# Kernel tuning notes

Hardware: AMD Instinct MI355X
Metric: run time of the kernel (lower is better)

Reference implementation:

```python
import jax, jax.numpy as jnp
import numpy as np

B, S, DMODEL, NHEAD = 2, 2048, 1024, 16
DK = DMODEL // NHEAD
INITRANGE = 0.1


def setup_inputs() -> dict:
    key = jax.random.key(0)
    kq, kk, kv, kwq, kwk, kwv, kwo = jax.random.split(key, 7)
    unif = lambda k, shape: jax.random.uniform(k, shape, jnp.float32, -INITRANGE, INITRANGE)
    return {
        "Q": jax.random.normal(kq, (B, S, DMODEL), jnp.float32),
        "K": jax.random.normal(kk, (B, S, DMODEL), jnp.float32),
        "V": jax.random.normal(kv, (B, S, DMODEL), jnp.float32),
        "WQ": unif(kwq, (NHEAD, DMODEL, DK)),
        "WK": unif(kwk, (NHEAD, DMODEL, DK)),
        "WV": unif(kwv, (NHEAD, DMODEL, DK)),
        "WO": unif(kwo, (NHEAD * DK, DMODEL)),
    }


def reference(Q, K, V, WQ, WK, WV, WO):
    dk = WQ.shape[-1]
    # per-head projections: [B,S,D] x [H,D,dk] -> [B,H,S,dk]
    Qi = jnp.einsum('bsd,hdk->bhsk', Q, WQ)
    Ki = jnp.einsum('bsd,hdk->bhsk', K, WK)
    Vi = jnp.einsum('bsd,hdk->bhsk', V, WV)
    scale = 1.0 / jnp.sqrt(jnp.asarray(dk, Qi.dtype))
    # full attention matrix [B,H,S,S] (faithful to the hand-rolled module; dropout in eval mode)
    attn = jax.nn.softmax(jnp.einsum('bhsk,bhtk->bhst', Qi, Ki) * scale, axis=-1)
    headi = jnp.einsum('bhst,bhtk->bhsk', attn, Vi)  # [B,H,S,dk]
    b, h, s, _ = headi.shape
    # NOTE: original does a raw reshape of contiguous (B,H,S,dk) -> (B,S,H*dk),
    # which mixes head and sequence axes in memory order. jnp row-major reshape
    # reproduces exactly the same element layout.
    out = headi.reshape(b, s, h * dk) @ WO  # [B,S,DMODEL]
    return out
```

## Files before the change

kernel.cpp:

```cpp
#include <hip/hip_runtime.h>
#include <hip/hip_bf16.h>
#include <stdint.h>

typedef unsigned short u16;
typedef unsigned int u32;
typedef __attribute__((ext_vector_type(4))) float f32x4;
typedef __attribute__((ext_vector_type(16))) float f32x16;
typedef __attribute__((ext_vector_type(8))) short bf16x8;
typedef __attribute__((ext_vector_type(4))) unsigned int u32x4;
typedef __attribute__((ext_vector_type(2))) unsigned int u32x2;

#define DEV __device__ __forceinline__

DEV u16 f2bf(float f) {
  union { float f; uint32_t u; } v; v.f = f;
  uint32_t u = v.u;
  return (u16)((u + 0x7fffu + ((u >> 16) & 1u)) >> 16);
}
DEV float bf2f(u16 h) {
  union { uint32_t u; float f; } v; v.u = ((uint32_t)h) << 16;
  return v.f;
}

DEV u32 cvtpk(float a, float b) {
  u32 r;
  asm("v_cvt_pk_bf16_f32 %0, %1, %2" : "=v"(r) : "v"(a), "v"(b));
  return r;
}

DEV void plswap(u32& a, u32& b) {
  asm("v_permlane32_swap_b32 %0, %1" : "+v"(a), "+v"(b));
}

DEV float fexp2(float x) {
  float r;
  asm("v_exp_f32 %0, %1" : "=v"(r) : "v"(x));
  return r;
}

DEV void gload_lds16(const u16* g, u16* l) {
  __builtin_amdgcn_global_load_lds(
      (const __attribute__((address_space(1))) void*)g,
      (__attribute__((address_space(3))) void*)l, 16, 0, 0);
}

__global__ __launch_bounds__(256) void prep_kernel(
    const float* __restrict__ Q, const float* __restrict__ K, const float* __restrict__ V,
    const float* __restrict__ WQ, const float* __restrict__ WK, const float* __restrict__ WV,
    const float* __restrict__ WO,
    u16* __restrict__ Qb, u16* __restrict__ Kb, u16* __restrict__ Vb,
    u16* __restrict__ Wt, u16* __restrict__ Wot) {
  const int i = blockIdx.x * 256 + threadIdx.x;
#pragma unroll
  for (int it = 0; it < 3; ++it) {
    int idx = it * 1048576 + i;
    int which = idx >> 20, j = idx & 1048575;
    const float* src = which == 0 ? Q : (which == 1 ? K : V);
    u16* dst = which == 0 ? Qb : (which == 1 ? Kb : Vb);
    float4 v = ((const float4*)src)[j];
    u32x2 pk;
    pk[0] = (u32)f2bf(v.x) | ((u32)f2bf(v.y) << 16);
    pk[1] = (u32)f2bf(v.z) | ((u32)f2bf(v.w) << 16);
    *(u32x2*)(dst + (size_t)j * 4) = pk;
  }
#pragma unroll
  for (int it = 0; it < 4; ++it) {
    int idx = it * 1048576 + i;
    if (idx < 3145728) {
      int p = idx >> 20, r = idx & 1048575;
      int n = r >> 10, d = r & 1023;
      int h = n >> 6, k = n & 63;
      const float* src = p == 0 ? WQ : (p == 1 ? WK : WV);
      Wt[idx] = f2bf(src[(h * 1024 + d) * 64 + k]);
    } else {
      int j = idx - 3145728;
      int c = j >> 10, k = j & 1023;
      Wot[j] = f2bf(WO[k * 1024 + c]);
    }
  }
}

template <int OUT_BF16>
__global__ __launch_bounds__(256, 2) void gemm_kernel(const u16* __restrict__ A,
                                                      const u16* __restrict__ Bt,
                                                      void* __restrict__ Cout) {
  __shared__ __align__(16) u16 Alds[128 * 64];
  __shared__ __align__(16) u16 Blds[128 * 64];
  const size_t zo = blockIdx.z;
  A += zo * 4194304;
  Bt += zo * 1048576;
  const int tid = threadIdx.x;
  const int l = tid & 63, w = tid >> 6;
  const int wm = w >> 1, wn = w & 1;
  const int d = blockIdx.x + 32 * blockIdx.y;
  const int orig = (d & 7) * 32 + (d >> 3);
  const int tileM = (orig & 31) * 128, tileN = (orig >> 5) * 128;
  const int lr = l >> 3, lch = l & 7;

  f32x4 acc[4][4] = {};

  for (int kt = 0; kt < 16; ++kt) {
    const int k0 = kt * 64;
#pragma unroll
    for (int i = 0; i < 4; ++i) {
      int r = i * 32 + w * 8 + lr;
      int sch = lch ^ (r & 7);
      gload_lds16(A + (size_t)(tileM + r) * 1024 + k0 + sch * 8, Alds + i * 2048 + w * 512);
      gload_lds16(Bt + (size_t)(tileN + r) * 1024 + k0 + sch * 8, Blds + i * 2048 + w * 512);
    }
    __syncthreads();
    bf16x8 af[4][2], bfr[4][2];
#pragma unroll
    for (int m = 0; m < 4; ++m) {
#pragma unroll
      for (int kk = 0; kk < 2; ++kk) {
        int row = wm * 64 + m * 16 + (l & 15);
        int ch = ((l >> 4) + kk * 4) ^ (row & 7);
        af[m][kk] = *(const bf16x8*)(Alds + row * 64 + ch * 8);
        int rowb = wn * 64 + m * 16 + (l & 15);
        int chb = ((l >> 4) + kk * 4) ^ (rowb & 7);
        bfr[m][kk] = *(const bf16x8*)(Blds + rowb * 64 + chb * 8);
      }
    }
#pragma unroll
    for (int m = 0; m < 4; ++m)
#pragma unroll
      for (int n = 0; n < 4; ++n)
#pragma unroll
        for (int kk = 0; kk < 2; ++kk)
          acc[m][n] = __builtin_amdgcn_mfma_f32_16x16x32_bf16(af[m][kk], bfr[n][kk], acc[m][n], 0, 0, 0);
    __syncthreads();
  }
#pragma unroll
  for (int m = 0; m < 4; ++m) {
    int row0 = tileM + wm * 64 + m * 16 + ((l >> 4) << 2);
#pragma unroll
    for (int n = 0; n < 4; ++n) {
      int col = tileN + wn * 64 + n * 16 + (l & 15);
#pragma unroll
      for (int q = 0; q < 4; ++q) {
        if (OUT_BF16)
          ((u16*)Cout)[zo * 4194304 + (size_t)(row0 + q) * 1024 + col] = f2bf(acc[m][n][q]);
        else
          ((float*)Cout)[(size_t)(row0 + q) * 1024 + col] = acc[m][n][q];
      }
    }
  }
}

__global__ __launch_bounds__(256) void transposeV_kernel(const u16* __restrict__ Vi,
                                                         u16* __restrict__ Vt) {
  __shared__ __align__(16) u16 tl[64][72];
  const int tid = threadIdx.x;
  const int st = blockIdx.x * 64;
  const int bh = blockIdx.y;
  const int b = bh >> 4, h = bh & 15;
#pragma unroll
  for (int i = 0; i < 2; ++i) {
    int idx = i * 256 + tid;
    int s = idx >> 3, ch = idx & 7;
    const u16* src = Vi + (size_t)(b * 2048 + st + s) * 1024 + h * 64 + ch * 8;
    u32x2 a = *(const u32x2*)src;
    u32x2 bb = *(const u32x2*)(src + 4);
    *(u32x2*)&tl[s][ch * 8] = a;
    *(u32x2*)&tl[s][ch * 8 + 4] = bb;
  }
  __syncthreads();
#pragma unroll
  for (int i = 0; i < 2; ++i) {
    int idx = i * 256 + tid;
    int dk = idx >> 3, ch = idx & 7;
    u32x4 outv;
    u16* tp = (u16*)&outv;
#pragma unroll
    for (int j = 0; j < 8; ++j) tp[j] = tl[ch * 8 + j][dk];
    *(u32x4*)(Vt + ((size_t)bh * 64 + dk) * 2048 + st + ch * 8) = outv;
  }
}

__global__ __launch_bounds__(256, 4) void attn_kernel(const u16* __restrict__ Qi,
                                                      const u16* __restrict__ Ki,
                                                      const u16* __restrict__ Vt,
                                                      u16* __restrict__ Op,
                                                      float* __restrict__ Lp) {
  __shared__ __align__(16) u16 Kl[2][4096];
  __shared__ __align__(16) u16 Vl[2][4096];
  const int tid = threadIdx.x;
  const int l = tid & 63, w = tid >> 6;
  const int lq = l & 31, hi = l >> 5;
  const int lr = l >> 3, lch = l & 7;
  const int dd = blockIdx.x;
  const int orig = (dd & 7) * 128 + (dd >> 3);
  const int bh = orig >> 5;
  const int rem = orig & 31;
  const int qb = rem >> 1, kvh = rem & 1;
  const int b = bh >> 4, h = bh & 15;
  const int qt = qb * 128 + w * 32;
  const int tb = kvh * 1024;

  const u16* Kbase = Ki + (size_t)b * 2048 * 1024 + h * 64;
  const u16* Vbase = Vt + (size_t)bh * 64 * 2048;

  bf16x8 qf[4];
  {
    const u16* qp = Qi + (size_t)(b * 2048 + qt + lq) * 1024 + h * 64 + hi * 8;
#pragma unroll
    for (int s = 0; s < 4; ++s) {
      u32x4 t4 = *(const u32x4*)(qp + s * 16);
      u16* tp = (u16*)&t4;
#pragma unroll
      for (int j = 0; j < 8; ++j) tp[j] = f2bf(bf2f(tp[j]) * 0.1803368867f);
      qf[s] = *(bf16x8*)&t4;
    }
  }

  f32x16 o0 = {}, o1 = {};
  float l_r = 0.f;

  auto STAGE = [&](int bb, int t) {
#pragma unroll
    for (int i = 0; i < 2; ++i) {
      int r = i * 32 + w * 8 + lr;
      int sch = lch ^ (r & 7);
      gload_lds16(Kbase + (size_t)(tb + t * 64 + r) * 1024 + sch * 8,
                  Kl[bb] + i * 2048 + w * 512);
      gload_lds16(Vbase + (size_t)r * 2048 + tb + t * 64 + sch * 8,
                  Vl[bb] + i * 2048 + w * 512);
    }
  };

  STAGE(0, 0);

#pragma unroll 2
  for (int tile = 0; tile < 16; ++tile) {
    const int cur = tile & 1;
    __syncthreads();
    if (tile + 1 < 16) STAGE(cur ^ 1, tile + 1);
    const u16* kl = Kl[cur];
    const u16* vl = Vl[cur];

    f32x16 s0 = {}, s1 = {};
    __builtin_amdgcn_s_setprio(1);
#pragma unroll
    for (int s = 0; s < 4; ++s) {
      int row = lq, c = s * 2 + hi;
      bf16x8 kf = *(const bf16x8*)(kl + row * 64 + (c ^ (row & 7)) * 8);
      s0 = __builtin_amdgcn_mfma_f32_32x32x16_bf16(kf, qf[s], s0, 0, 0, 0);
    }
#pragma unroll
    for (int s = 0; s < 4; ++s) {
      int row = 32 + lq, c = s * 2 + hi;
      bf16x8 kf = *(const bf16x8*)(kl + row * 64 + (c ^ (row & 7)) * 8);
      s1 = __builtin_amdgcn_mfma_f32_32x32x16_bf16(kf, qf[s], s1, 0, 0, 0);
    }
    __builtin_amdgcn_s_setprio(0);

    float rs = 0.f;
    bf16x8 pa[4];
#pragma unroll
    for (int s4 = 0; s4 < 4; ++s4) {
      const int rb = 8 * (s4 & 1);
      float p[8];
#pragma unroll
      for (int j = 0; j < 8; ++j) {
        float sv = (s4 < 2) ? ((const float*)&s0)[rb + j] : ((const float*)&s1)[rb + j];
        p[j] = fexp2(sv);
      }
      rs += ((p[0] + p[1]) + (p[2] + p[3])) + ((p[4] + p[5]) + (p[6] + p[7]));
      u32 w10 = cvtpk(p[0], p[1]);
      u32 w11 = cvtpk(p[2], p[3]);
      u32 w20 = cvtpk(p[4], p[5]);
      u32 w21 = cvtpk(p[6], p[7]);
      plswap(w10, w20);
      plswap(w11, w21);
      u32x4 af;
      af[0] = w10;
      af[1] = w11;
      af[2] = w20;
      af[3] = w21;
      pa[s4] = *(bf16x8*)&af;
    }
    rs += __shfl_xor(rs, 32, 64);
    l_r += rs;

    __builtin_amdgcn_s_setprio(1);
#pragma unroll
    for (int s4 = 0; s4 < 4; ++s4) {
      int rowd = lq, c = s4 * 2 + hi;
      bf16x8 vf = *(const bf16x8*)(vl + rowd * 64 + (c ^ (rowd & 7)) * 8);
      o0 = __builtin_amdgcn_mfma_f32_32x32x16_bf16(pa[s4], vf, o0, 0, 0, 0);
    }
#pragma unroll
    for (int s4 = 0; s4 < 4; ++s4) {
      int rowd = 32 + lq, c = s4 * 2 + hi;
      bf16x8 vf = *(const bf16x8*)(vl + rowd * 64 + (c ^ (rowd & 7)) * 8);
      o1 = __builtin_amdgcn_mfma_f32_32x32x16_bf16(pa[s4], vf, o1, 0, 0, 0);
    }
    __builtin_amdgcn_s_setprio(0);
  }

#pragma unroll
  for (int r = 0; r < 16; ++r) {
    int qr = (r & 3) + 8 * (r >> 2) + 4 * hi;
    u16* hp = Op + (size_t)kvh * 4194304 + ((size_t)bh * 2048 + qt + qr) * 64;
    hp[lq] = f2bf(o0[r]);
    hp[32 + lq] = f2bf(o1[r]);
  }
  if (hi == 0) Lp[(size_t)kvh * 65536 + (size_t)bh * 2048 + qt + lq] = l_r;
}

__global__ __launch_bounds__(256) void combine_kernel(const u16* __restrict__ Op,
                                                      const float* __restrict__ Lp,
                                                      u16* __restrict__ Hd) {
  const int idx = blockIdx.x * 256 + threadIdx.x;
  const int g = idx >> 3, j = idx & 7;
  const float fac = 1.f / (Lp[g] + Lp[65536 + g]);
  const u16* a = Op + (size_t)g * 64 + j * 8;
  const u16* bptr = a + 4194304;
  u32x4 va = *(const u32x4*)a;
  u32x4 vb = *(const u32x4*)bptr;
  const u16* pa = (const u16*)&va;
  const u16* pb = (const u16*)&vb;
  u32x4 outv;
  u16* po = (u16*)&outv;
#pragma unroll
  for (int e = 0; e < 8; ++e) po[e] = f2bf((bf2f(pa[e]) + bf2f(pb[e])) * fac);
  *(u32x4*)(Hd + (size_t)g * 64 + j * 8) = outv;
}

extern "C" void kernel_launch(void* const* d_in, const int* in_sizes, int n_in,
                              void* d_out, int out_size, void* d_ws, size_t ws_size,
                              hipStream_t stream) {
  const float* Q = (const float*)d_in[0];
  const float* K = (const float*)d_in[1];
  const float* V = (const float*)d_in[2];
  const float* WQ = (const float*)d_in[3];
  const float* WK = (const float*)d_in[4];
  const float* WV = (const float*)d_in[5];
  const float* WO = (const float*)d_in[6];
  float* out = (float*)d_out;

  size_t off = 0;
  char* ws = (char*)d_ws;
  auto nxt = [&](size_t n) { void* p = ws + off; off += (n + 255) & ~(size_t)255; return p; };
  u16* Qb = (u16*)nxt(3ull * 4096 * 1024 * 2);
  u16* Qi = (u16*)nxt(3ull * 4096 * 1024 * 2);
  u16* Vtb = (u16*)nxt(4096ull * 1024 * 2);
  u16* Hd = (u16*)nxt(4096ull * 1024 * 2);
  u16* Wt = (u16*)nxt(3ull * 1048576 * 2);
  u16* Wot = (u16*)nxt(1048576ull * 2);
  u16* Ki = Qi + 4194304;
  u16* Vi = Qi + 2 * 4194304;
  u16* Op = Qb;
  float* Lp = (float*)(Qb + 2ull * 4194304);

  prep_kernel<<<4096, 256, 0, stream>>>(Q, K, V, WQ, WK, WV, WO, Qb, Qb + 4194304,
                                        Qb + 2 * 4194304, Wt, Wot);

  gemm_kernel<1><<<dim3(32, 8, 3), 256, 0, stream>>>(Qb, Wt, Qi);

  transposeV_kernel<<<dim3(32, 32), 256, 0, stream>>>(Vi, Vtb);

  attn_kernel<<<1024, 256, 0, stream>>>(Qi, Ki, Vtb, Op, Lp);

  combine_kernel<<<2048, 256, 0, stream>>>(Op, Lp, Hd);

  gemm_kernel<0><<<dim3(32, 8, 1), 256, 0, stream>>>(Hd, Wot, out);
}
```

Baseline: 140.0 us.

## Split attention KV range four ways and tile weight transposes through LDS

The attention kernel now splits each query block's key range into four chunks instead of two, which doubles the grid to 2048 blocks for more parallelism. The fourth partial output goes into the Hd buffer and Lp moves to its own workspace region. The combine kernel now sums four partials. Weight conversion and transposition move out of the prep kernel into a separate LDS-tiled transpose kernel, replacing the strided, uncoalesced gathers. The cost is extra partial-output traffic in combine and one more kernel launch.

```diff
diff --git a/kernel.cpp b/kernel.cpp
--- a/kernel.cpp
+++ b/kernel.cpp
@@ -46,10 +46,7 @@
 
 __global__ __launch_bounds__(256) void prep_kernel(
     const float* __restrict__ Q, const float* __restrict__ K, const float* __restrict__ V,
-    const float* __restrict__ WQ, const float* __restrict__ WK, const float* __restrict__ WV,
-    const float* __restrict__ WO,
-    u16* __restrict__ Qb, u16* __restrict__ Kb, u16* __restrict__ Vb,
-    u16* __restrict__ Wt, u16* __restrict__ Wot) {
+    u16* __restrict__ Qb, u16* __restrict__ Kb, u16* __restrict__ Vb) {
   const int i = blockIdx.x * 256 + threadIdx.x;
 #pragma unroll
   for (int it = 0; it < 3; ++it) {
@@ -63,20 +60,55 @@
     pk[1] = (u32)f2bf(v.z) | ((u32)f2bf(v.w) << 16);
     *(u32x2*)(dst + (size_t)j * 4) = pk;
   }
-#pragma unroll
-  for (int it = 0; it < 4; ++it) {
-    int idx = it * 1048576 + i;
-    if (idx < 3145728) {
-      int p = idx >> 20, r = idx & 1048575;
-      int n = r >> 10, d = r & 1023;
-      int h = n >> 6, k = n & 63;
-      const float* src = p == 0 ? WQ : (p == 1 ? WK : WV);
-      Wt[idx] = f2bf(src[(h * 1024 + d) * 64 + k]);
-    } else {
-      int j = idx - 3145728;
-      int c = j >> 10, k = j & 1023;
-      Wot[j] = f2bf(WO[k * 1024 + c]);
-    }
+}
+
+__global__ __launch_bounds__(256) void transposeW_kernel(
+    const float* __restrict__ WQ, const float* __restrict__ WK, const float* __restrict__ WV,
+    const float* __restrict__ WO, u16* __restrict__ Wt, u16* __restrict__ Wot) {
+  __shared__ __align__(16) u16 tl[64][72];
+  const int tid = threadIdx.x;
+  const int bid = blockIdx.x;
+  const float* src;
+  u16* dst;
+  int rstride;
+  if (bid < 768) {
+    int p = bid >> 8, rest = bid & 255;
+    int h = rest >> 4, dt = rest & 15;
+    const float* W = p == 0 ? WQ : (p == 1 ? WK : WV);
+    src = W + (size_t)(h * 1024 + dt * 64) * 64;
+    dst = Wt + (size_t)p * 1048576 + (size_t)h * 64 * 1024 + dt * 64;
+    rstride = 64;
+  } else {
+    int idx2 = bid - 768;
+    int kt = idx2 >> 4, ct = idx2 & 15;
+    src = WO + (size_t)kt * 64 * 1024 + ct * 64;
+    dst = Wot + (size_t)ct * 64 * 1024 + kt * 64;
+    rstride = 1024;
+  }
+#pragma unroll
+  for (int i = 0; i < 2; ++i) {
+    int idx = i * 256 + tid;
+    int row = idx >> 3, c8 = idx & 7;
+    const float* sp = src + (size_t)row * rstride + c8 * 8;
+    float4 a = *(const float4*)sp;
+    float4 b = *(const float4*)(sp + 4);
+    u32x4 pk;
+    pk[0] = (u32)f2bf(a.x) | ((u32)f2bf(a.y) << 16);
+    pk[1] = (u32)f2bf(a.z) | ((u32)f2bf(a.w) << 16);
+    pk[2] = (u32)f2bf(b.x) | ((u32)f2bf(b.y) << 16);
+    pk[3] = (u32)f2bf(b.z) | ((u32)f2bf(b.w) << 16);
+    *(u32x4*)&tl[row][c8 * 8] = pk;
+  }
+  __syncthreads();
+#pragma unroll
+  for (int i = 0; i < 2; ++i) {
+    int idx = i * 256 + tid;
+    int row2 = idx >> 3, s8 = idx & 7;
+    u32x4 outv;
+    u16* tp = (u16*)&outv;
+#pragma unroll
+    for (int j = 0; j < 8; ++j) tp[j] = tl[s8 * 8 + j][row2];
+    *(u32x4*)(dst + (size_t)row2 * 1024 + s8 * 8) = outv;
   }
 }
 
@@ -182,6 +214,7 @@
                                                       const u16* __restrict__ Ki,
                                                       const u16* __restrict__ Vt,
                                                       u16* __restrict__ Op,
+                                                      u16* __restrict__ Op3,
                                                       float* __restrict__ Lp) {
   __shared__ __align__(16) u16 Kl[2][4096];
   __shared__ __align__(16) u16 Vl[2][4096];
@@ -190,13 +223,13 @@
   const int lq = l & 31, hi = l >> 5;
   const int lr = l >> 3, lch = l & 7;
   const int dd = blockIdx.x;
-  const int orig = (dd & 7) * 128 + (dd >> 3);
-  const int bh = orig >> 5;
-  const int rem = orig & 31;
-  const int qb = rem >> 1, kvh = rem & 1;
+  const int orig = (dd & 7) * 256 + (dd >> 3);
+  const int bh = orig >> 6;
+  const int rem = orig & 63;
+  const int qb = rem >> 2, kvh = rem & 3;
   const int b = bh >> 4, h = bh & 15;
   const int qt = qb * 128 + w * 32;
-  const int tb = kvh * 1024;
+  const int tb = kvh * 512;
 
   const u16* Kbase = Ki + (size_t)b * 2048 * 1024 + h * 64;
   const u16* Vbase = Vt + (size_t)bh * 64 * 2048;
@@ -232,10 +265,10 @@
   STAGE(0, 0);
 
 #pragma unroll 2
-  for (int tile = 0; tile < 16; ++tile) {
+  for (int tile = 0; tile < 8; ++tile) {
     const int cur = tile & 1;
     __syncthreads();
-    if (tile + 1 < 16) STAGE(cur ^ 1, tile + 1);
+    if (tile + 1 < 8) STAGE(cur ^ 1, tile + 1);
     const u16* kl = Kl[cur];
     const u16* vl = Vl[cur];
 
@@ -299,10 +332,11 @@
     __builtin_amdgcn_s_setprio(0);
   }
 
+  u16* opb = (kvh == 3) ? Op3 : (Op + (size_t)kvh * 4194304);
 #pragma unroll
   for (int r = 0; r < 16; ++r) {
     int qr = (r & 3) + 8 * (r >> 2) + 4 * hi;
-    u16* hp = Op + (size_t)kvh * 4194304 + ((size_t)bh * 2048 + qt + qr) * 64;
+    u16* hp = opb + ((size_t)bh * 2048 + qt + qr) * 64;
     hp[lq] = f2bf(o0[r]);
     hp[32 + lq] = f2bf(o1[r]);
   }
@@ -314,18 +348,23 @@
                                                       u16* __restrict__ Hd) {
   const int idx = blockIdx.x * 256 + threadIdx.x;
   const int g = idx >> 3, j = idx & 7;
-  const float fac = 1.f / (Lp[g] + Lp[65536 + g]);
-  const u16* a = Op + (size_t)g * 64 + j * 8;
-  const u16* bptr = a + 4194304;
-  u32x4 va = *(const u32x4*)a;
-  u32x4 vb = *(const u32x4*)bptr;
-  const u16* pa = (const u16*)&va;
-  const u16* pb = (const u16*)&vb;
+  const float fac =
+      1.f / (Lp[g] + Lp[65536 + g] + Lp[131072 + g] + Lp[196608 + g]);
+  const size_t off = (size_t)g * 64 + j * 8;
+  u32x4 v0 = *(const u32x4*)(Op + off);
+  u32x4 v1 = *(const u32x4*)(Op + 4194304 + off);
+  u32x4 v2 = *(const u32x4*)(Op + 2ull * 4194304 + off);
+  u32x4 v3 = *(const u32x4*)(Hd + off);
+  const u16* p0 = (const u16*)&v0;
+  const u16* p1 = (const u16*)&v1;
+  const u16* p2 = (const u16*)&v2;
+  const u16* p3 = (const u16*)&v3;
   u32x4 outv;
   u16* po = (u16*)&outv;
 #pragma unroll
-  for (int e = 0; e < 8; ++e) po[e] = f2bf((bf2f(pa[e]) + bf2f(pb[e])) * fac);
-  *(u32x4*)(Hd + (size_t)g * 64 + j * 8) = outv;
+  for (int e = 0; e < 8; ++e)
+    po[e] = f2bf((bf2f(p0[e]) + bf2f(p1[e]) + bf2f(p2[e]) + bf2f(p3[e])) * fac);
+  *(u32x4*)(Hd + off) = outv;
 }
 
 extern "C" void kernel_launch(void* const* d_in, const int* in_sizes, int n_in,
@@ -349,19 +388,20 @@
   u16* Hd = (u16*)nxt(4096ull * 1024 * 2);
   u16* Wt = (u16*)nxt(3ull * 1048576 * 2);
   u16* Wot = (u16*)nxt(1048576ull * 2);
+  float* Lp = (float*)nxt(4ull * 65536 * 4);
   u16* Ki = Qi + 4194304;
   u16* Vi = Qi + 2 * 4194304;
   u16* Op = Qb;
-  float* Lp = (float*)(Qb + 2ull * 4194304);
-
-  prep_kernel<<<4096, 256, 0, stream>>>(Q, K, V, WQ, WK, WV, WO, Qb, Qb + 4194304,
-                                        Qb + 2 * 4194304, Wt, Wot);
+
+  prep_kernel<<<4096, 256, 0, stream>>>(Q, K, V, Qb, Qb + 4194304, Qb + 2 * 4194304);
+
+  transposeW_kernel<<<1024, 256, 0, stream>>>(WQ, WK, WV, WO, Wt, Wot);
 
   gemm_kernel<1><<<dim3(32, 8, 3), 256, 0, stream>>>(Qb, Wt, Qi);
 
   transposeV_kernel<<<dim3(32, 32), 256, 0, stream>>>(Vi, Vtb);
 
-  attn_kernel<<<1024, 256, 0, stream>>>(Qi, Ki, Vtb, Op, Lp);
+  attn_kernel<<<2048, 256, 0, stream>>>(Qi, Ki, Vtb, Op, Hd, Lp);
 
   combine_kernel<<<2048, 256, 0, stream>>>(Op, Lp, Hd);
 
```

Result: faster. 137.1 us (-2.1%).
